# Performance work log

Hardware: AMD Instinct MI355X
Metric: run time of the kernel (lower is better)

Reference implementation:

```python
import jax, jax.numpy as jnp
import numpy as np

B = 32; N_NODES = 1000; WINDOW = 4; D = 128; N_PARTS = 10
T = 2; T_INT = 1; T_TEMP = 1
N_TOTAL = B * WINDOW * N_NODES
E_INT = 200000; E_TEMP = 96000


def setup_inputs() -> dict:
    key = jax.random.key(0)
    ks = jax.random.split(key, 24)
    inp = {}
    inp["node_inputs"] = jax.random.randint(ks[0], (B, N_NODES), 0, 10)
    inp["node_indices"] = jax.random.randint(ks[1], (E_INT,), 0, N_TOTAL)
    inp["neighbour_indices"] = jax.random.randint(ks[2], (E_INT,), 0, N_TOTAL)
    inp["temp_node_indices"] = jax.random.randint(ks[3], (E_TEMP,), 0, N_TOTAL)
    inp["temp_neighbour_indices"] = jax.random.randint(ks[4], (E_TEMP,), 0, N_TOTAL)

    def dense(k, din, dout):
        return jax.random.normal(k, (din, dout), jnp.float32) * np.float32(1.0 / np.sqrt(din))

    inp["embed_table"] = jax.random.normal(ks[5], (10, D), jnp.float32)
    # message MLP: 2*D -> 64 -> 64 -> 64 -> 64 -> D (4 gelu hidden, linear out)
    inp["msg_W_in"] = dense(ks[6], 2 * D, 64); inp["msg_b_in"] = jnp.zeros((64,), jnp.float32)
    inp["msg_W_hid"] = jax.random.normal(ks[7], (3, 64, 64), jnp.float32) * np.float32(1.0 / 8.0)
    inp["msg_b_hid"] = jnp.zeros((3, 64), jnp.float32)
    inp["msg_W_out"] = dense(ks[8], 64, D); inp["msg_b_out"] = jnp.zeros((D,), jnp.float32)
    # readout MLP: D -> 64 -> 64 -> 64 -> 64 -> n_parts
    inp["ro_W_in"] = dense(ks[9], D, 64); inp["ro_b_in"] = jnp.zeros((64,), jnp.float32)
    inp["ro_W_hid"] = jax.random.normal(ks[10], (3, 64, 64), jnp.float32) * np.float32(1.0 / 8.0)
    inp["ro_b_hid"] = jnp.zeros((3, 64), jnp.float32)
    inp["ro_W_out"] = dense(ks[11], 64, N_PARTS); inp["ro_b_out"] = jnp.zeros((N_PARTS,), jnp.float32)
    # GRU cells (tf.keras reset_after=True): kernel [D,3D], recurrent [D,3D], input+recurrent biases
    for nm, base in (("gi", 12), ("gt", 16)):
        inp[nm + "_Wx"] = dense(ks[base], D, 3 * D)
        inp[nm + "_Wh"] = dense(ks[base + 1], D, 3 * D)
        inp[nm + "_bi"] = jnp.zeros((3 * D,), jnp.float32)
        inp[nm + "_br"] = jnp.zeros((3 * D,), jnp.float32)
    return inp


def _mlp(x, W_in, b_in, W_hid, b_hid, W_out, b_out):
    h = jax.nn.gelu(x @ W_in + b_in, approximate=False)
    for i in range(W_hid.shape[0]):
        h = jax.nn.gelu(h @ W_hid[i] + b_hid[i], approximate=False)
    return h @ W_out + b_out


def _gru(h, x, Wx, Wh, bi, br):
    # tf.keras GRUCell, reset_after=True
    xz, xr, xh = jnp.split(x @ Wx + bi, 3, axis=1)
    hz, hr, hh = jnp.split(h @ Wh + br, 3, axis=1)
    z = jax.nn.sigmoid(xz + hz)
    r = jax.nn.sigmoid(xr + hr)
    cand = jnp.tanh(xh + r * hh)
    return z * h + (1.0 - z) * cand


def _message_mean(h, ni, bi, msg_p):
    g0 = h[ni]              # [E, D] node gather
    g1 = h[bi]              # [E, D] neighbour gather
    x = jnp.concatenate([jnp.concatenate([g0, g1], 1), jnp.concatenate([g1, g0], 1)], 0)  # [2E, 2D]
    msg = _mlp(x, *msg_p)   # [2E, D]
    seg = jnp.concatenate([bi, ni], 0)
    s = jax.ops.segment_sum(msg, seg, num_segments=h.shape[0])
    c = jax.ops.segment_sum(jnp.ones((seg.shape[0], 1), msg.dtype), seg, num_segments=h.shape[0])
    return s / jnp.maximum(c, 1.0)


def reference(node_inputs, node_indices, neighbour_indices, temp_node_indices, temp_neighbour_indices,
              embed_table, msg_W_in, msg_b_in, msg_W_hid, msg_b_hid, msg_W_out, msg_b_out,
              ro_W_in, ro_b_in, ro_W_hid, ro_b_hid, ro_W_out, ro_b_out,
              gi_Wx, gi_Wh, gi_bi, gi_br, gt_Wx, gt_Wh, gt_bi, gt_br):
    msg_p = (msg_W_in, msg_b_in, msg_W_hid, msg_b_hid, msg_W_out, msg_b_out)
    h = embed_table[node_inputs]                       # [B, N, D]
    h = jnp.repeat(h, WINDOW, axis=0).reshape(-1, D)   # [B*W*N, D]
    for _ in range(T):
        for _ in range(T_INT):
            m = _message_mean(h, node_indices, neighbour_indices, msg_p)
            h = _gru(h, m, gi_Wx, gi_Wh, gi_bi, gi_br)
        for _ in range(T_TEMP):
            m = _message_mean(h, temp_node_indices, temp_neighbour_indices, msg_p)
            h = _gru(h, m, gt_Wx, gt_Wh, gt_bi, gt_br)
    ridx = jnp.arange(N_NODES)[None, :] + jnp.arange(B)[:, None] * (WINDOW * N_NODES)
    return _mlp(h[ridx], ro_W_in, ro_b_in, ro_W_hid, ro_b_hid, ro_W_out, ro_b_out)  # [B, N, n_parts]
```

## Files before the change

kernel.cpp:

```cpp
#include <hip/hip_runtime.h>
#include <math.h>


#define DDIM 128
#define NTOT 128000
#define HBYTES 65536000ULL
#define EBLK 128

typedef unsigned short u16;
using f32x4 = __attribute__((ext_vector_type(4))) float;
using s16x8 = __attribute__((ext_vector_type(8))) short;

__device__ __forceinline__ float fast_rcp(float x) {
    return __builtin_amdgcn_rcpf(x);
}
__device__ __forceinline__ float gelu_fast(float x) {
    const float ax = fabsf(x) * 0.70710678118654752440f;
    const float t  = fast_rcp(1.0f + 0.3275911f * ax);
    const float poly = t * (0.254829592f + t * (-0.284496736f +
                       t * (1.421413741f + t * (-1.453152027f +
                       t * 1.061405429f))));
    const float e = __expf(-ax * ax);
    const float erfax = 1.0f - poly * e;
    const float erfv = copysignf(erfax, x);
    return 0.5f * x * (1.0f + erfv);
}
__device__ __forceinline__ float sigmoid_fast(float x) {
    return fast_rcp(1.0f + __expf(-x));
}
__device__ __forceinline__ float tanh_fast(float x) {
    const float e = __expf(2.0f * x);
    return 1.0f - 2.0f * fast_rcp(e + 1.0f);
}
__device__ __forceinline__ u16 f2bf(float x) {
    unsigned u = __float_as_uint(x);
    u += 0x7fffu + ((u >> 16) & 1u);
    return (u16)(u >> 16);
}
__device__ __forceinline__ float bf2f(u16 h) {
    return __uint_as_float(((unsigned)h) << 16);
}

__global__ __launch_bounds__(256) void embed_kernel(
    const int* __restrict__ inp, const float* __restrict__ table,
    float* __restrict__ h)
{
    int gid = blockIdx.x * 256 + threadIdx.x;
    if (gid >= NTOT * 32) return;
    int row = gid >> 5;
    int q   = gid & 31;
    int b   = row / 4000;
    int n   = (row % 4000) % 1000;
    int e   = inp[b * 1000 + n];
    ((float4*)h)[gid] = ((const float4*)table)[e * 32 + q];
}

__global__ __launch_bounds__(256) void hist_kernel(
    const int* __restrict__ ni, const int* __restrict__ bi, int E,
    int* __restrict__ deg)
{
    int g = blockIdx.x * 256 + threadIdx.x;
    if (g < E)          atomicAdd(&deg[bi[g]], 1);
    else if (g < 2 * E) atomicAdd(&deg[ni[g - E]], 1);
}

__global__ __launch_bounds__(256) void blockscan_kernel(
    const int* __restrict__ deg, int* __restrict__ offp, int* __restrict__ bsum)
{
    __shared__ int s[256];
    int tid = threadIdx.x;
    int i = blockIdx.x * 256 + tid;
    int v = deg[i];
    s[tid] = v;
    __syncthreads();
    for (int off = 1; off < 256; off <<= 1) {
        int t = (tid >= off) ? s[tid - off] : 0;
        __syncthreads();
        s[tid] += t;
        __syncthreads();
    }
    offp[i] = s[tid] - v;
    if (tid == 255) bsum[blockIdx.x] = s[255];
}

__global__ __launch_bounds__(512) void bscan_kernel(
    const int* __restrict__ bsum, int* __restrict__ bexc, int nb)
{
    __shared__ int s[512];
    int t = threadIdx.x;
    int v = (t < nb) ? bsum[t] : 0;
    s[t] = v;
    __syncthreads();
    for (int off = 1; off < 512; off <<= 1) {
        int u = (t >= off) ? s[t - off] : 0;
        __syncthreads();
        s[t] += u;
        __syncthreads();
    }
    if (t < nb) bexc[t] = s[t] - v;
}

__global__ __launch_bounds__(256) void fill_kernel(
    const int* __restrict__ ni, const int* __restrict__ bi, int E,
    const int* __restrict__ offp, const int* __restrict__ bexc,
    int* __restrict__ cursor, int* __restrict__ elist, int* __restrict__ slotseg)
{
    int g = blockIdx.x * 256 + threadIdx.x;
    if (g >= 2 * E) return;
    int seg = (g < E) ? bi[g] : ni[g - E];
    int pos = atomicAdd(&cursor[seg], 1);
    int slot = offp[seg] + bexc[seg >> 8] + pos;
    elist[slot] = g;
    slotseg[slot] = seg;
}

__global__ __launch_bounds__(256) void straddle_kernel(
    const int* __restrict__ slotseg, int nblocks32,
    int* __restrict__ list, int* __restrict__ count)
{
    int b = blockIdx.x * 256 + threadIdx.x + 1;
    if (b >= nblocks32) return;
    int s = slotseg[b * 32];
    if (s >= 0 && slotseg[b * 32 - 1] == s) {
        int pos = atomicAdd(count, 1);
        list[pos] = s;
    }
}

__global__ __launch_bounds__(64) void zero_rows_kernel(
    const int* __restrict__ list, const int* __restrict__ count,
    float* __restrict__ sbuf)
{
    int i = blockIdx.x;
    if (i >= *count) return;
    int seg = list[i];
    float4* row = (float4*)(sbuf + (size_t)seg * 64);
    if (threadIdx.x < 16) row[threadIdx.x] = make_float4(0.f, 0.f, 0.f, 0.f);
}


__global__ __launch_bounds__(256) void pack_gateBx_kernel(
    const float* __restrict__ Wout, const float* __restrict__ Wx,
    u16* __restrict__ BH, u16* __restrict__ BL)
{
    int idx = blockIdx.x * 256 + threadIdx.x;
    if (idx >= 24576) return;
    int j    = idx & 7;
    int lane = (idx >> 3) & 63;
    int tile = idx >> 9;
    int nt   = tile & 7;
    int g    = (tile >> 3) % 3;
    int kt   = tile / 24;
    int k   = kt * 32 + (lane >> 4) * 8 + j;
    int col = g * 128 + nt * 16 + (lane & 15);
    float acc = 0.0f;
    for (int t = 0; t < 128; ++t)
        acc = fmaf(Wout[k * 128 + t], Wx[t * 384 + col], acc);
    u16 hb = f2bf(acc);
    BH[idx] = hb;
    BL[idx] = f2bf(acc - bf2f(hb));
}

__global__ __launch_bounds__(256) void pack_gateBh_kernel(
    const float* __restrict__ Wh, u16* __restrict__ BH, u16* __restrict__ BL)
{
    int idx = blockIdx.x * 256 + threadIdx.x;
    if (idx >= 49152) return;
    int j    = idx & 7;
    int lane = (idx >> 3) & 63;
    int tile = idx >> 9;
    int nt   = tile & 7;
    int s    = (tile >> 3) % 3;
    int kt   = tile / 24;
    int k    = kt * 32 + (lane >> 4) * 8 + j;
    int col  = ((s == 2) ? 256 : s * 128) + nt * 16 + (lane & 15);
    float v = Wh[k * 384 + col];
    u16 hb = f2bf(v);
    BH[idx] = hb;
    BL[idx] = f2bf(v - bf2f(hb));
}

__global__ __launch_bounds__(256) void pack_gbias_kernel(
    const float* __restrict__ bout, const float* __restrict__ Wx,
    float* __restrict__ bc)
{
    int n = blockIdx.x * 256 + threadIdx.x;
    if (n >= 384) return;
    float acc = 0.0f;
    for (int t = 0; t < 128; ++t)
        acc = fmaf(bout[t], Wx[t * 384 + n], acc);
    bc[n] = acc;
}

__global__ __launch_bounds__(256) void pack_preB_kernel(
    const float* __restrict__ Win, u16* __restrict__ BH, u16* __restrict__ BL)
{
    int idx = blockIdx.x * 256 + threadIdx.x;
    if (idx >= 16384) return;
    int j    = idx & 7;
    int lane = (idx >> 3) & 63;
    int nt2  = (idx >> 9) & 7;
    int kt2  = idx >> 12;
    int k = kt2 * 32 + (lane >> 4) * 8 + j;
    int n = nt2 * 16 + (lane & 15);
    float v = (n < 64) ? Win[k * 64 + n] : Win[(128 + k) * 64 + (n - 64)];
    u16 hb = f2bf(v);
    BH[idx] = hb;
    BL[idx] = f2bf(v - bf2f(hb));
}

__global__ __launch_bounds__(256) void pack_hidB_kernel(
    const float* __restrict__ Whid, u16* __restrict__ BH, u16* __restrict__ BL)
{
    int idx = blockIdx.x * 256 + threadIdx.x;
    if (idx >= 12288) return;
    int j    = idx & 7;
    int lane = (idx >> 3) & 63;
    int nt   = (idx >> 9) & 3;
    int kt   = (idx >> 11) & 1;
    int L    = idx >> 12;
    int k = kt * 32 + (lane >> 4) * 8 + j;
    int n = nt * 16 + (lane & 15);
    float v = Whid[L * 4096 + k * 64 + n];
    u16 hb = f2bf(v);
    BH[idx] = hb;
    BL[idx] = f2bf(v - bf2f(hb));
}

__global__ __launch_bounds__(512, 2) void node_pre_mfma(
    const float* __restrict__ h,
    const u16* __restrict__ BpH, const u16* __restrict__ BpL,
    const float* __restrict__ binp, float* __restrict__ pout)
{
    __shared__ short sm[32768];
    const int tid  = threadIdx.x;
    const int lane = tid & 63;
    const int w    = tid >> 6;
    const int jg   = w & 1;
    const int mh   = w >> 1;
    const int nbase = blockIdx.x * 128;

    const int mS = tid >> 2, q = tid & 3;
    const int nodeS = nbase + mS;
    const int laneS = (mS & 15) + 16 * q;
    const int seg_m = mS >> 4;

    #pragma unroll
    for (int c = 0; c < 4; ++c) {
        const int kl = c * 32 + q * 8;
        const float* src = h + (size_t)nodeS * DDIM + kl;
        const float4 v0 = ((const float4*)src)[0];
        const float4 v1 = ((const float4*)src)[1];
        float xv[8] = { v0.x, v0.y, v0.z, v0.w, v1.x, v1.y, v1.z, v1.w };
        s16x8 hi8, lo8;
        #pragma unroll
        for (int i = 0; i < 8; ++i) {
            u16 hb = f2bf(xv[i]);
            hi8[i] = (short)hb;
            lo8[i] = (short)f2bf(xv[i] - bf2f(hb));
        }
        const int off = (c * 8 + seg_m) * 512 + laneS * 8;
        *(s16x8*)(sm + off)         = hi8;
        *(s16x8*)(sm + off + 16384) = lo8;
    }
    __syncthreads();

    f32x4 acc2[2][4];
    #pragma unroll
    for (int mf = 0; mf < 2; ++mf)
        #pragma unroll
        for (int t4 = 0; t4 < 4; ++t4)
            acc2[mf][t4] = (f32x4){0.f, 0.f, 0.f, 0.f};

    const s16x8* Ph8 = (const s16x8*)BpH;
    const s16x8* Pl8 = (const s16x8*)BpL;
    #pragma unroll
    for (int kt2 = 0; kt2 < 4; ++kt2) {
        const int a0off = (kt2 * 8 + 2 * mh) * 512 + lane * 8;
        const s16x8 aH0 = *(const s16x8*)(sm + a0off);
        const s16x8 aL0 = *(const s16x8*)(sm + 16384 + a0off);
        const s16x8 aH1 = *(const s16x8*)(sm + a0off + 512);
        const s16x8 aL1 = *(const s16x8*)(sm + 16384 + a0off + 512);
        #pragma unroll
        for (int t4 = 0; t4 < 4; ++t4) {
            const int idx = (kt2 * 8 + jg * 4 + t4) * 64 + lane;
            const s16x8 bH = Ph8[idx];
            const s16x8 bL = Pl8[idx];
            acc2[0][t4] = __builtin_amdgcn_mfma_f32_16x16x32_bf16(aH0, bH, acc2[0][t4], 0, 0, 0);
            acc2[0][t4] = __builtin_amdgcn_mfma_f32_16x16x32_bf16(aH0, bL, acc2[0][t4], 0, 0, 0);
            acc2[0][t4] = __builtin_amdgcn_mfma_f32_16x16x32_bf16(aL0, bH, acc2[0][t4], 0, 0, 0);
            acc2[1][t4] = __builtin_amdgcn_mfma_f32_16x16x32_bf16(aH1, bH, acc2[1][t4], 0, 0, 0);
            acc2[1][t4] = __builtin_amdgcn_mfma_f32_16x16x32_bf16(aH1, bL, acc2[1][t4], 0, 0, 0);
            acc2[1][t4] = __builtin_amdgcn_mfma_f32_16x16x32_bf16(aL1, bH, acc2[1][t4], 0, 0, 0);
        }
    }
    #pragma unroll
    for (int mf = 0; mf < 2; ++mf) {
        const int mtile = 2 * mh + mf;
        #pragma unroll
        for (int t4 = 0; t4 < 4; ++t4) {
            const int n = jg * 64 + t4 * 16 + (lane & 15);
            const float badd = (n < 64) ? binp[n] : 0.0f;
            #pragma unroll
            for (int r = 0; r < 4; ++r) {
                const int m = mtile * 16 + (lane >> 4) * 4 + r;
                pout[(size_t)(nbase + m) * DDIM + n] = acc2[mf][t4][r] + badd;
            }
        }
    }
}

__global__ __launch_bounds__(512) void edge_mlp_mfma(
    const int* __restrict__ ni, const int* __restrict__ bi, int E,
    const int* __restrict__ elist, const int* __restrict__ slotseg,
    const float* __restrict__ p,
    const u16* __restrict__ BhH, const u16* __restrict__ BhL,
    const float* __restrict__ bhid,
    float* __restrict__ sbuf)
{
    __shared__ short smA[17408];
    __shared__ int   segLDS[EBLK];
    __shared__ int   segedge[2];
    float* scat = (float*)smA;

    const int tid  = threadIdx.x;
    const int lane = tid & 63;
    const int w    = tid >> 6;
    const int s0   = blockIdx.x * EBLK;

    if (tid < 128) segLDS[tid] = slotseg[s0 + tid];
    if (tid == 0) segedge[0] = slotseg[s0 - 1];
    if (tid == 1) segedge[1] = slotseg[s0 + EBLK];

    {
        const int m  = (tid & 15) | (w << 4);
        const int gg = (tid >> 4) & 3;
        const int slot = s0 + m;
        const int g = elist[slot];
        int first, second;
        if (g < E) { first = ni[g];     second = bi[g];     }
        else       { first = bi[g - E]; second = ni[g - E]; }
        #pragma unroll
        for (int kt = 0; kt < 2; ++kt) {
            const int k0 = kt * 32 + gg * 8;
            const float4* pa = (const float4*)(p + (size_t)first  * DDIM + k0);
            const float4* pb = (const float4*)(p + (size_t)second * DDIM + 64 + k0);
            const float4 a0 = pa[0], a1 = pa[1], b0 = pb[0], b1 = pb[1];
            float x[8] = { a0.x + b0.x, a0.y + b0.y, a0.z + b0.z, a0.w + b0.w,
                           a1.x + b1.x, a1.y + b1.y, a1.z + b1.z, a1.w + b1.w };
            s16x8 hi8, lo8;
            #pragma unroll
            for (int j = 0; j < 8; ++j) {
                const float v = gelu_fast(x[j]);
                u16 hb = f2bf(v);
                hi8[j] = (short)hb;
                lo8[j] = (short)f2bf(v - bf2f(hb));
            }
            const int off = (kt * 8 + w) * 512 + lane * 8;
            *(s16x8*)(smA + off)        = hi8;
            *(s16x8*)(smA + 8192 + off) = lo8;
        }
    }

    const int mt = w;
    for (int L = 0; L < 2; ++L) {
        f32x4 acc[4];
        #pragma unroll
        for (int nt = 0; nt < 4; ++nt) {
            const float bv = bhid[L * 64 + nt * 16 + (lane & 15)];
            acc[nt] = (f32x4){bv, bv, bv, bv};
        }
        #pragma unroll
        for (int kt = 0; kt < 2; ++kt) {
            const s16x8 aH = *(const s16x8*)(smA + (kt * 8 + mt) * 512 + lane * 8);
            const s16x8 aL = *(const s16x8*)(smA + 8192 + (kt * 8 + mt) * 512 + lane * 8);
            #pragma unroll
            for (int nt = 0; nt < 4; ++nt) {
                const int bidx = (L * 8 + kt * 4 + nt) * 64 + lane;
                const s16x8 bH = ((const s16x8*)BhH)[bidx];
                const s16x8 bL = ((const s16x8*)BhL)[bidx];
                acc[nt] = __builtin_amdgcn_mfma_f32_16x16x32_bf16(aH, bH, acc[nt], 0, 0, 0);
                acc[nt] = __builtin_amdgcn_mfma_f32_16x16x32_bf16(aH, bL, acc[nt], 0, 0, 0);
                acc[nt] = __builtin_amdgcn_mfma_f32_16x16x32_bf16(aL, bH, acc[nt], 0, 0, 0);
            }
        }
        #pragma unroll
        for (int nt = 0; nt < 4; ++nt) {
            #pragma unroll
            for (int r = 0; r < 4; ++r) {
                const float v = gelu_fast(acc[nt][r]);
                const int ml  = (lane >> 4) * 4 + r;
                const int k   = nt * 16 + (lane & 15);
                const int kt2 = k >> 5, gg = (k >> 3) & 3, j = k & 7;
                const int off = (kt2 * 8 + mt) * 512 + (ml + 16 * gg) * 8 + j;
                u16 hb = f2bf(v);
                smA[off]        = (short)hb;
                smA[8192 + off] = (short)f2bf(v - bf2f(hb));
            }
        }
    }

    float gl[4][4];
    {
        f32x4 acc[4];
        #pragma unroll
        for (int nt = 0; nt < 4; ++nt) {
            const float bv = bhid[2 * 64 + nt * 16 + (lane & 15)];
            acc[nt] = (f32x4){bv, bv, bv, bv};
        }
        #pragma unroll
        for (int kt = 0; kt < 2; ++kt) {
            const s16x8 aH = *(const s16x8*)(smA + (kt * 8 + mt) * 512 + lane * 8);
            const s16x8 aL = *(const s16x8*)(smA + 8192 + (kt * 8 + mt) * 512 + lane * 8);
            #pragma unroll
            for (int nt = 0; nt < 4; ++nt) {
                const int bidx = (2 * 8 + kt * 4 + nt) * 64 + lane;
                const s16x8 bH = ((const s16x8*)BhH)[bidx];
                const s16x8 bL = ((const s16x8*)BhL)[bidx];
                acc[nt] = __builtin_amdgcn_mfma_f32_16x16x32_bf16(aH, bH, acc[nt], 0, 0, 0);
                acc[nt] = __builtin_amdgcn_mfma_f32_16x16x32_bf16(aH, bL, acc[nt], 0, 0, 0);
                acc[nt] = __builtin_amdgcn_mfma_f32_16x16x32_bf16(aL, bH, acc[nt], 0, 0, 0);
            }
        }
        #pragma unroll
        for (int nt = 0; nt < 4; ++nt)
            #pragma unroll
            for (int r = 0; r < 4; ++r)
                gl[nt][r] = gelu_fast(acc[nt][r]);
    }

    __syncthreads();
    #pragma unroll
    for (int nt = 0; nt < 4; ++nt)
        #pragma unroll
        for (int r = 0; r < 4; ++r)
            scat[(mt * 16 + (lane >> 4) * 4 + r) * 68 + nt * 16 + (lane & 15)]
                = gl[nt][r];
    __syncthreads();

    if (tid < 256) {
        const int col = tid & 63;
        const int r0  = (tid >> 6) * 32;
        const int r1  = r0 + 32;
        int   runSeg = -2;
        float runacc = 0.0f;
        bool  leftC  = true;
        for (int rowi = r0; rowi < r1; ++rowi) {
            const int sg = segLDS[rowi];
            const float v = scat[rowi * 68 + col];
            if (sg != runSeg) {
                if (runSeg >= 0) {
                    float* pp = sbuf + (size_t)runSeg * 64 + col;
                    if (leftC) *pp = runacc;
                    else       atomicAdd(pp, runacc);
                }
                runSeg = sg;
                runacc = v;
                if (rowi == r0) {
                    const int prev = (rowi == 0) ? segedge[0] : segLDS[rowi - 1];
                    leftC = (prev != sg);
                } else {
                    leftC = true;
                }
            } else {
                runacc += v;
            }
        }
        if (runSeg >= 0) {
            const int nxt = (r1 == 128) ? segedge[1] : segLDS[r1];
            const bool rightC = (nxt != runSeg);
            float* pp = sbuf + (size_t)runSeg * 64 + col;
            if (leftC && rightC) *pp = runacc;
            else                 atomicAdd(pp, runacc);
        }
    }
}

__global__ __launch_bounds__(256, 3) void gru_mfma_kernel(
    float* __restrict__ hio, const float* __restrict__ Ssum,
    const int* __restrict__ deg,
    const u16* __restrict__ BxH, const u16* __restrict__ BxL,
    const u16* __restrict__ BhH, const u16* __restrict__ BhL,
    const float* __restrict__ bc,
    const float* __restrict__ bi_, const float* __restrict__ br_,
    const u16* __restrict__ BpH, const u16* __restrict__ BpL,
    const float* __restrict__ binp,
    float* __restrict__ pout)
{
    __shared__ short sm[16384];
    const int tid  = threadIdx.x;
    const int lane = tid & 63;
    const int w    = tid >> 6;
    const int jg   = w & 1;
    const int mh   = w >> 1;
    const int nbase = blockIdx.x * 64;

    const int mS = tid >> 2, q = tid & 3;
    const int nodeS = nbase + mS;
    const int laneS = (mS & 15) + 16 * q;
    const int seg_m = mS >> 4;
    const int dg = deg[nodeS];
    const float ci = (dg > 0) ? fast_rcp((float)dg) : 0.0f;

    #pragma unroll
    for (int c = 0; c < 2; ++c) {
        const int kl = c * 32 + q * 8;
        const float* src = Ssum + (size_t)nodeS * 64 + kl;
        const float4 v0 = ((const float4*)src)[0];
        const float4 v1 = ((const float4*)src)[1];
        float xv[8] = { v0.x * ci, v0.y * ci, v0.z * ci, v0.w * ci,
                        v1.x * ci, v1.y * ci, v1.z * ci, v1.w * ci };
        s16x8 hi8, lo8;
        #pragma unroll
        for (int i = 0; i < 8; ++i) {
            u16 hb = f2bf(xv[i]);
            hi8[i] = (short)hb;
            lo8[i] = (short)f2bf(xv[i] - bf2f(hb));
        }
        const int off = (c * 4 + seg_m) * 512 + laneS * 8;
        *(s16x8*)(sm + off)        = hi8;
        *(s16x8*)(sm + off + 8192) = lo8;
    }
    __syncthreads();

    f32x4 acc[2][4][4];
    #pragma unroll
    for (int mf = 0; mf < 2; ++mf)
        #pragma unroll
        for (int g = 0; g < 4; ++g)
            #pragma unroll
            for (int t4 = 0; t4 < 4; ++t4)
                acc[mf][g][t4] = (f32x4){0.f, 0.f, 0.f, 0.f};

    {
        const s16x8* Bx8 = (const s16x8*)BxH;
        const s16x8* Bxl8 = (const s16x8*)BxL;
        #pragma unroll
        for (int kt = 0; kt < 2; ++kt) {
            const int a0off = (kt * 4 + 2 * mh) * 512 + lane * 8;
            const s16x8 aH0 = *(const s16x8*)(sm + a0off);
            const s16x8 aL0 = *(const s16x8*)(sm + 8192 + a0off);
            const s16x8 aH1 = *(const s16x8*)(sm + a0off + 512);
            const s16x8 aL1 = *(const s16x8*)(sm + 8192 + a0off + 512);
            #pragma unroll
            for (int g = 0; g < 3; ++g) {
                #pragma unroll
                for (int t4 = 0; t4 < 4; ++t4) {
                    const int idx = (kt * 24 + g * 8 + jg * 4 + t4) * 64 + lane;
                    const s16x8 bH = Bx8[idx];
                    const s16x8 bL = Bxl8[idx];
                    acc[0][g][t4] = __builtin_amdgcn_mfma_f32_16x16x32_bf16(aH0, bH, acc[0][g][t4], 0, 0, 0);
                    acc[0][g][t4] = __builtin_amdgcn_mfma_f32_16x16x32_bf16(aH0, bL, acc[0][g][t4], 0, 0, 0);
                    acc[0][g][t4] = __builtin_amdgcn_mfma_f32_16x16x32_bf16(aL0, bH, acc[0][g][t4], 0, 0, 0);
                    acc[1][g][t4] = __builtin_amdgcn_mfma_f32_16x16x32_bf16(aH1, bH, acc[1][g][t4], 0, 0, 0);
                    acc[1][g][t4] = __builtin_amdgcn_mfma_f32_16x16x32_bf16(aH1, bL, acc[1][g][t4], 0, 0, 0);
                    acc[1][g][t4] = __builtin_amdgcn_mfma_f32_16x16x32_bf16(aL1, bH, acc[1][g][t4], 0, 0, 0);
                }
            }
        }
    }
    __syncthreads();

    #pragma unroll
    for (int c = 0; c < 4; ++c) {
        const int kl = c * 32 + q * 8;
        const float* src = hio + (size_t)nodeS * DDIM + kl;
        const float4 v0 = ((const float4*)src)[0];
        const float4 v1 = ((const float4*)src)[1];
        float xv[8] = { v0.x, v0.y, v0.z, v0.w, v1.x, v1.y, v1.z, v1.w };
        s16x8 hi8, lo8;
        #pragma unroll
        for (int i = 0; i < 8; ++i) {
            u16 hb = f2bf(xv[i]);
            hi8[i] = (short)hb;
            lo8[i] = (short)f2bf(xv[i] - bf2f(hb));
        }
        const int off = (c * 4 + seg_m) * 512 + laneS * 8;
        *(s16x8*)(sm + off)        = hi8;
        *(s16x8*)(sm + off + 8192) = lo8;
    }
    __syncthreads();

    {
        const s16x8* Bh8 = (const s16x8*)BhH;
        const s16x8* Bhl8 = (const s16x8*)BhL;
        #pragma unroll
        for (int kt = 0; kt < 4; ++kt) {
            const int a0off = (kt * 4 + 2 * mh) * 512 + lane * 8;
            const s16x8 aH0 = *(const s16x8*)(sm + a0off);
            const s16x8 aL0 = *(const s16x8*)(sm + 8192 + a0off);
            const s16x8 aH1 = *(const s16x8*)(sm + a0off + 512);
            const s16x8 aL1 = *(const s16x8*)(sm + 8192 + a0off + 512);
            #pragma unroll
            for (int s = 0; s < 3; ++s) {
                const int g = (s == 2) ? 3 : s;
                #pragma unroll
                for (int t4 = 0; t4 < 4; ++t4) {
                    const int idx = (kt * 24 + s * 8 + jg * 4 + t4) * 64 + lane;
                    const s16x8 bH = Bh8[idx];
                    const s16x8 bL = Bhl8[idx];
                    acc[0][g][t4] = __builtin_amdgcn_mfma_f32_16x16x32_bf16(aH0, bH, acc[0][g][t4], 0, 0, 0);
                    acc[0][g][t4] = __builtin_amdgcn_mfma_f32_16x16x32_bf16(aH0, bL, acc[0][g][t4], 0, 0, 0);
                    acc[0][g][t4] = __builtin_amdgcn_mfma_f32_16x16x32_bf16(aL0, bH, acc[0][g][t4], 0, 0, 0);
                    acc[1][g][t4] = __builtin_amdgcn_mfma_f32_16x16x32_bf16(aH1, bH, acc[1][g][t4], 0, 0, 0);
                    acc[1][g][t4] = __builtin_amdgcn_mfma_f32_16x16x32_bf16(aH1, bL, acc[1][g][t4], 0, 0, 0);
                    acc[1][g][t4] = __builtin_amdgcn_mfma_f32_16x16x32_bf16(aL1, bH, acc[1][g][t4], 0, 0, 0);
                }
            }
        }
    }

    bool bon[2][4];
    #pragma unroll
    for (int mf = 0; mf < 2; ++mf)
        #pragma unroll
        for (int r = 0; r < 4; ++r)
            bon[mf][r] = deg[nbase + (2 * mh + mf) * 16 + (lane >> 4) * 4 + r] > 0;

    float hn[2][4][4];
    #pragma unroll
    for (int t4 = 0; t4 < 4; ++t4) {
        const int j = jg * 64 + t4 * 16 + (lane & 15);
        const float b_az = bi_[j]       + br_[j];
        const float b_ar = bi_[128 + j] + br_[128 + j];
        const float b_xh = bi_[256 + j];
        const float b_hh = br_[256 + j];
        const float bcz = bc[j];
        const float bcr = bc[128 + j];
        const float bcx = bc[256 + j];
        const int jbase = (j >> 5) * 2048 + ((j >> 3) & 3) * 128 + (j & 7);
        #pragma unroll
        for (int mf = 0; mf < 2; ++mf) {
            const int mtile = 2 * mh + mf;
            #pragma unroll
            for (int r = 0; r < 4; ++r) {
                const int m15 = (lane >> 4) * 4 + r;
                const int off = jbase + mtile * 512 + m15 * 8;
                const float hv = bf2f((u16)sm[off]) + bf2f((u16)sm[8192 + off]);
                const int m = mtile * 16 + m15;
                const float bsel = bon[mf][r] ? 1.0f : 0.0f;
                const float az = acc[mf][0][t4][r] + b_az + bsel * bcz;
                const float ar = acc[mf][1][t4][r] + b_ar + bsel * bcr;
                const float xh = acc[mf][2][t4][r] + b_xh + bsel * bcx;
                const float hh = acc[mf][3][t4][r] + b_hh;
                const float z    = sigmoid_fast(az);
                const float rr   = sigmoid_fast(ar);
                const float cand = tanh_fast(xh + rr * hh);
                const float v    = z * hv + (1.0f - z) * cand;
                hio[(size_t)(nbase + m) * DDIM + j] = v;
                hn[mf][t4][r] = v;
            }
        }
    }
    __syncthreads();

    #pragma unroll
    for (int mf = 0; mf < 2; ++mf) {
        const int mtile = 2 * mh + mf;
        #pragma unroll
        for (int t4 = 0; t4 < 4; ++t4) {
            #pragma unroll
            for (int r = 0; r < 4; ++r) {
                const int m15 = (lane >> 4) * 4 + r;
                const int j   = jg * 64 + t4 * 16 + (lane & 15);
                const int kt2 = j >> 5, gg = (j >> 3) & 3, jj = j & 7;
                const int off = (kt2 * 4 + mtile) * 512 + (m15 + 16 * gg) * 8 + jj;
                const float v = hn[mf][t4][r];
                u16 hb = f2bf(v);
                sm[off]        = (short)hb;
                sm[off + 8192] = (short)f2bf(v - bf2f(hb));
            }
        }
    }
    __syncthreads();

    f32x4 acc2[2][4];
    #pragma unroll
    for (int mf = 0; mf < 2; ++mf)
        #pragma unroll
        for (int t4 = 0; t4 < 4; ++t4)
            acc2[mf][t4] = (f32x4){0.f, 0.f, 0.f, 0.f};

    const s16x8* Ph8 = (const s16x8*)BpH;
    const s16x8* Pl8 = (const s16x8*)BpL;
    #pragma unroll
    for (int kt2 = 0; kt2 < 4; ++kt2) {
        const int a0off = (kt2 * 4 + 2 * mh) * 512 + lane * 8;
        const s16x8 aH0 = *(const s16x8*)(sm + a0off);
        const s16x8 aL0 = *(const s16x8*)(sm + 8192 + a0off);
        const s16x8 aH1 = *(const s16x8*)(sm + a0off + 512);
        const s16x8 aL1 = *(const s16x8*)(sm + 8192 + a0off + 512);
        #pragma unroll
        for (int t4 = 0; t4 < 4; ++t4) {
            const int idx = (kt2 * 8 + jg * 4 + t4) * 64 + lane;
            const s16x8 bH = Ph8[idx];
            const s16x8 bL = Pl8[idx];
            acc2[0][t4] = __builtin_amdgcn_mfma_f32_16x16x32_bf16(aH0, bH, acc2[0][t4], 0, 0, 0);
            acc2[0][t4] = __builtin_amdgcn_mfma_f32_16x16x32_bf16(aH0, bL, acc2[0][t4], 0, 0, 0);
            acc2[0][t4] = __builtin_amdgcn_mfma_f32_16x16x32_bf16(aL0, bH, acc2[0][t4], 0, 0, 0);
            acc2[1][t4] = __builtin_amdgcn_mfma_f32_16x16x32_bf16(aH1, bH, acc2[1][t4], 0, 0, 0);
            acc2[1][t4] = __builtin_amdgcn_mfma_f32_16x16x32_bf16(aH1, bL, acc2[1][t4], 0, 0, 0);
            acc2[1][t4] = __builtin_amdgcn_mfma_f32_16x16x32_bf16(aL1, bH, acc2[1][t4], 0, 0, 0);
        }
    }
    #pragma unroll
    for (int mf = 0; mf < 2; ++mf) {
        const int mtile = 2 * mh + mf;
        #pragma unroll
        for (int t4 = 0; t4 < 4; ++t4) {
            const int n = jg * 64 + t4 * 16 + (lane & 15);
            const float badd = (n < 64) ? binp[n] : 0.0f;
            #pragma unroll
            for (int r = 0; r < 4; ++r) {
                const int m = mtile * 16 + (lane >> 4) * 4 + r;
                pout[(size_t)(nbase + m) * DDIM + n] = acc2[mf][t4][r] + badd;
            }
        }
    }
}

__global__ __launch_bounds__(64) void readout_kernel(
    const float* __restrict__ h,
    const float* __restrict__ Win,  const float* __restrict__ bin,
    const float* __restrict__ Whid, const float* __restrict__ bhid,
    const float* __restrict__ Wout, const float* __restrict__ bout,
    float* __restrict__ out)
{
    __shared__ float xs[64 * 65];
    const int tid = threadIdx.x;
    const int row = blockIdx.x * 64 + tid;
    const int b = row / 1000, n = row % 1000;
    const float4* xrow = (const float4*)(h + ((size_t)b * 4000 + n) * DDIM);

    {
        float acc[64];
        #pragma unroll
        for (int j = 0; j < 64; ++j) acc[j] = bin[j];
        #pragma unroll 2
        for (int k4 = 0; k4 < 32; ++k4) {
            float4 xv = xrow[k4];
            #pragma unroll
            for (int kk = 0; kk < 4; ++kk) {
                const float xk = (&xv.x)[kk];
                const float* wr = Win + (size_t)(k4 * 4 + kk) * 64;
                #pragma unroll
                for (int j = 0; j < 64; ++j) acc[j] = fmaf(xk, wr[j], acc[j]);
            }
        }
        #pragma unroll
        for (int j = 0; j < 64; ++j) xs[tid * 65 + j] = gelu_fast(acc[j]);
    }

    for (int L = 0; L < 3; ++L) {
        float acc[64];
        #pragma unroll
        for (int j = 0; j < 64; ++j) acc[j] = bhid[L * 64 + j];
        #pragma unroll 4
        for (int k = 0; k < 64; ++k) {
            const float xk = xs[tid * 65 + k];
            const float* wr = Whid + (size_t)L * 4096 + (size_t)k * 64;
            #pragma unroll
            for (int j = 0; j < 64; ++j) acc[j] = fmaf(xk, wr[j], acc[j]);
        }
        #pragma unroll
        for (int j = 0; j < 64; ++j) xs[tid * 65 + j] = gelu_fast(acc[j]);
    }

    float acc[10];
    #pragma unroll
    for (int pj = 0; pj < 10; ++pj) acc[pj] = bout[pj];
    #pragma unroll 4
    for (int k = 0; k < 64; ++k) {
        const float xk = xs[tid * 65 + k];
        const float* wr = Wout + k * 10;
        #pragma unroll
        for (int pj = 0; pj < 10; ++pj) acc[pj] = fmaf(xk, wr[pj], acc[pj]);
    }
    #pragma unroll
    for (int pj = 0; pj < 10; ++pj) out[(size_t)row * 10 + pj] = acc[pj];
}

extern "C" void kernel_launch(void* const* d_in, const int* in_sizes, int n_in,
                              void* d_out, int out_size, void* d_ws, size_t ws_size,
                              hipStream_t stream) {
    const int*   node_inputs = (const int*)d_in[0];
    const int*   ni_int = (const int*)d_in[1];
    const int*   bi_int = (const int*)d_in[2];
    const int*   ni_tmp = (const int*)d_in[3];
    const int*   bi_tmp = (const int*)d_in[4];
    const float* embed  = (const float*)d_in[5];
    const float* mWin   = (const float*)d_in[6];
    const float* mbin   = (const float*)d_in[7];
    const float* mWhid  = (const float*)d_in[8];
    const float* mbhid  = (const float*)d_in[9];
    const float* mWout  = (const float*)d_in[10];
    const float* mbout  = (const float*)d_in[11];
    const float* roWin  = (const float*)d_in[12];
    const float* robin  = (const float*)d_in[13];
    const float* roWhid = (const float*)d_in[14];
    const float* robhid = (const float*)d_in[15];
    const float* roWout = (const float*)d_in[16];
    const float* robout = (const float*)d_in[17];
    const float* giWx = (const float*)d_in[18];
    const float* giWh = (const float*)d_in[19];
    const float* gibi = (const float*)d_in[20];
    const float* gibr = (const float*)d_in[21];
    const float* gtWx = (const float*)d_in[22];
    const float* gtWh = (const float*)d_in[23];
    const float* gtbi = (const float*)d_in[24];
    const float* gtbr = (const float*)d_in[25];
    float* out = (float*)d_out;

    const int E_INT = 200000, E_TMP = 96000;
    const int NSLOT_I = 400000;
    const int NSLOT_T = 192000;
    const int NBLK_I = NSLOT_I / EBLK;
    const int NBLK_T = NSLOT_T / EBLK;
    const int NS32_I = NSLOT_I / 32;
    const int NS32_T = NSLOT_T / 32;

    char* ws = (char*)d_ws;
    float* B0 = (float*)(ws);
    float* B1 = (float*)(ws + HBYTES);
    float* B2 = (float*)(ws + 2 * HBYTES);
    char*  ib = ws + 3 * HBYTES;

    int* deg_i   = (int*)(ib);
    int* deg_t   = (int*)(ib + 512000);
    int* offp_i  = (int*)(ib + 1024000);
    int* offp_t  = (int*)(ib + 1536000);
    int* bexc_i  = (int*)(ib + 2048000);
    int* bexc_t  = (int*)(ib + 2052096);
    int* bsum    = (int*)(ib + 2056192);
    int* cursor  = (int*)(ib + 2060288);
    int* el_i    = (int*)(ib + 2572288);
    int* el_t    = (int*)(ib + 4172288);
    int* ssi_raw = (int*)(ib + 4940288);
    int* sst_raw = (int*)(ib + 6540296);
    char* fb = ib + 8114176;
    u16* BxiH = (u16*)(fb);
    u16* BxiL = (u16*)(fb +  49152);
    u16* BhiH = (u16*)(fb +  98304);
    u16* BhiL = (u16*)(fb + 196608);
    u16* BxtH = (u16*)(fb + 294912);
    u16* BxtL = (u16*)(fb + 344064);
    u16* BhtH = (u16*)(fb + 393216);
    u16* BhtL = (u16*)(fb + 491520);
    float* bci = (float*)(fb + 589824);
    float* bct = (float*)(fb + 591360);
    u16* BpH  = (u16*)(fb + 592896);
    u16* BpL  = (u16*)(fb + 625664);
    u16* EhH  = (u16*)(fb + 658432);
    u16* EhL  = (u16*)(fb + 683008);
    int* str_i  = (int*)(fb + 707584);
    int* str_t  = (int*)(fb + 757584);
    int* strc_i = (int*)(fb + 781584);
    int* strc_t = (int*)(fb + 781588);
    int* ssi = ssi_raw + 1;
    int* sst = sst_raw + 1;

    embed_kernel<<<16000, 256, 0, stream>>>(node_inputs, embed, B0);

    hipMemsetAsync(deg_i, 0, NTOT * sizeof(int), stream);
    hipMemsetAsync(deg_t, 0, NTOT * sizeof(int), stream);
    hist_kernel<<<(2 * E_INT + 255) / 256, 256, 0, stream>>>(ni_int, bi_int, E_INT, deg_i);
    hist_kernel<<<(2 * E_TMP + 255) / 256, 256, 0, stream>>>(ni_tmp, bi_tmp, E_TMP, deg_t);

    hipMemsetAsync(ssi_raw, 0xFF, (size_t)(NSLOT_I + 2) * sizeof(int), stream);
    hipMemsetAsync(sst_raw, 0xFF, (size_t)(NSLOT_T + 2) * sizeof(int), stream);

    blockscan_kernel<<<500, 256, 0, stream>>>(deg_i, offp_i, bsum);
    bscan_kernel<<<1, 512, 0, stream>>>(bsum, bexc_i, 500);
    hipMemsetAsync(cursor, 0, NTOT * sizeof(int), stream);
    fill_kernel<<<(2 * E_INT + 255) / 256, 256, 0, stream>>>(
        ni_int, bi_int, E_INT, offp_i, bexc_i, cursor, el_i, ssi);

    blockscan_kernel<<<500, 256, 0, stream>>>(deg_t, offp_t, bsum);
    bscan_kernel<<<1, 512, 0, stream>>>(bsum, bexc_t, 500);
    hipMemsetAsync(cursor, 0, NTOT * sizeof(int), stream);
    fill_kernel<<<(2 * E_TMP + 255) / 256, 256, 0, stream>>>(
        ni_tmp, bi_tmp, E_TMP, offp_t, bexc_t, cursor, el_t, sst);

    hipMemsetAsync(strc_i, 0, sizeof(int), stream);
    hipMemsetAsync(strc_t, 0, sizeof(int), stream);
    straddle_kernel<<<(NS32_I + 255) / 256, 256, 0, stream>>>(ssi, NS32_I, str_i, strc_i);
    straddle_kernel<<<(NS32_T + 255) / 256, 256, 0, stream>>>(sst, NS32_T, str_t, strc_t);

    pack_gateBx_kernel<<<96, 256, 0, stream>>>(mWout, giWx, BxiH, BxiL);
    pack_gateBx_kernel<<<96, 256, 0, stream>>>(mWout, gtWx, BxtH, BxtL);
    pack_gateBh_kernel<<<192, 256, 0, stream>>>(giWh, BhiH, BhiL);
    pack_gateBh_kernel<<<192, 256, 0, stream>>>(gtWh, BhtH, BhtL);
    pack_gbias_kernel<<<2, 256, 0, stream>>>(mbout, giWx, bci);
    pack_gbias_kernel<<<2, 256, 0, stream>>>(mbout, gtWx, bct);
    pack_preB_kernel<<<64, 256, 0, stream>>>(mWin, BpH, BpL);
    pack_hidB_kernel<<<48, 256, 0, stream>>>(mWhid, EhH, EhL);

    node_pre_mfma<<<NTOT / 128, 512, 0, stream>>>(B0, BpH, BpL, mbin, B1);

    for (int ph = 0; ph < 4; ++ph) {
        const bool isInt = (ph % 2 == 0);
        if (isInt) {
            zero_rows_kernel<<<NS32_I, 64, 0, stream>>>(str_i, strc_i, B2);
            edge_mlp_mfma<<<NBLK_I, 512, 0, stream>>>(
                ni_int, bi_int, E_INT, el_i, ssi, B1,
                EhH, EhL, mbhid, B2);
            gru_mfma_kernel<<<NTOT / 64, 256, 0, stream>>>(
                B0, B2, deg_i, BxiH, BxiL, BhiH, BhiL, bci,
                gibi, gibr, BpH, BpL, mbin, B1);
        } else {
            zero_rows_kernel<<<NS32_T, 64, 0, stream>>>(str_t, strc_t, B2);
            edge_mlp_mfma<<<NBLK_T, 512, 0, stream>>>(
                ni_tmp, bi_tmp, E_TMP, el_t, sst, B1,
                EhH, EhL, mbhid, B2);
            gru_mfma_kernel<<<NTOT / 64, 256, 0, stream>>>(
                B0, B2, deg_t, BxtH, BxtL, BhtH, BhtL, bct,
                gtbi, gtbr, BpH, BpL, mbin, B1);
        }
    }

    readout_kernel<<<500, 64, 0, stream>>>(
        B0, roWin, robin, roWhid, robhid, roWout, robout, out);
}
```

Before: 1.253 ms.

## Merge first half of recurrent GEMM into input phase and stage output through LDS

The GRU kernel now loads the first half of the hidden state together with the message sums, so the first MFMA phase also runs the first two K-tiles of the recurrent GEMM. The second phase handles only the remaining two K-tiles, and the gate epilogue picks the LDS region by column group. This overlaps more global loads with compute and shortens the serialized second load-and-sync phase. The projection output is also written to a padded LDS tile and stored as row-contiguous float4s rather than scattered scalar stores, at the cost of an extra barrier and slightly more shared memory.

Measured after the change: 1.314 ms. +4.9%, slower.

```diff
diff --git a/kernel.cpp b/kernel.cpp
--- a/kernel.cpp
+++ b/kernel.cpp
@@ -487,7 +487,7 @@
     const float* __restrict__ binp,
     float* __restrict__ pout)
 {
-    __shared__ short sm[16384];
+    __shared__ short sm[16768];
     const int tid  = threadIdx.x;
     const int lane = tid & 63;
     const int w    = tid >> 6;
@@ -502,24 +502,46 @@
     const int dg = deg[nodeS];
     const float ci = (dg > 0) ? fast_rcp((float)dg) : 0.0f;
 
-    #pragma unroll
-    for (int c = 0; c < 2; ++c) {
-        const int kl = c * 32 + q * 8;
-        const float* src = Ssum + (size_t)nodeS * 64 + kl;
-        const float4 v0 = ((const float4*)src)[0];
-        const float4 v1 = ((const float4*)src)[1];
-        float xv[8] = { v0.x * ci, v0.y * ci, v0.z * ci, v0.w * ci,
-                        v1.x * ci, v1.y * ci, v1.z * ci, v1.w * ci };
-        s16x8 hi8, lo8;
-        #pragma unroll
-        for (int i = 0; i < 8; ++i) {
-            u16 hb = f2bf(xv[i]);
-            hi8[i] = (short)hb;
-            lo8[i] = (short)f2bf(xv[i] - bf2f(hb));
-        }
-        const int off = (c * 4 + seg_m) * 512 + laneS * 8;
-        *(s16x8*)(sm + off)        = hi8;
-        *(s16x8*)(sm + off + 8192) = lo8;
+    {
+        float4 sv[4], hv0[4];
+        #pragma unroll
+        for (int c = 0; c < 2; ++c) {
+            const int kl = c * 32 + q * 8;
+            sv[c * 2]     = ((const float4*)(Ssum + (size_t)nodeS * 64 + kl))[0];
+            sv[c * 2 + 1] = ((const float4*)(Ssum + (size_t)nodeS * 64 + kl))[1];
+            hv0[c * 2]     = ((const float4*)(hio + (size_t)nodeS * DDIM + kl))[0];
+            hv0[c * 2 + 1] = ((const float4*)(hio + (size_t)nodeS * DDIM + kl))[1];
+        }
+        #pragma unroll
+        for (int c = 0; c < 2; ++c) {
+            float xv[8] = { sv[c*2].x * ci, sv[c*2].y * ci, sv[c*2].z * ci, sv[c*2].w * ci,
+                            sv[c*2+1].x * ci, sv[c*2+1].y * ci, sv[c*2+1].z * ci, sv[c*2+1].w * ci };
+            s16x8 hi8, lo8;
+            #pragma unroll
+            for (int i = 0; i < 8; ++i) {
+                u16 hb = f2bf(xv[i]);
+                hi8[i] = (short)hb;
+                lo8[i] = (short)f2bf(xv[i] - bf2f(hb));
+            }
+            const int off = (c * 4 + seg_m) * 512 + laneS * 8;
+            *(s16x8*)(sm + off)        = hi8;
+            *(s16x8*)(sm + off + 8192) = lo8;
+        }
+        #pragma unroll
+        for (int c = 0; c < 2; ++c) {
+            float xv[8] = { hv0[c*2].x, hv0[c*2].y, hv0[c*2].z, hv0[c*2].w,
+                            hv0[c*2+1].x, hv0[c*2+1].y, hv0[c*2+1].z, hv0[c*2+1].w };
+            s16x8 hi8, lo8;
+            #pragma unroll
+            for (int i = 0; i < 8; ++i) {
+                u16 hb = f2bf(xv[i]);
+                hi8[i] = (short)hb;
+                lo8[i] = (short)f2bf(xv[i] - bf2f(hb));
+            }
+            const int off = 4096 + (c * 4 + seg_m) * 512 + laneS * 8;
+            *(s16x8*)(sm + off)        = hi8;
+            *(s16x8*)(sm + off + 8192) = lo8;
+        }
     }
     __syncthreads();
 
@@ -535,34 +557,61 @@
     {
         const s16x8* Bx8 = (const s16x8*)BxH;
         const s16x8* Bxl8 = (const s16x8*)BxL;
+        const s16x8* Bh8 = (const s16x8*)BhH;
+        const s16x8* Bhl8 = (const s16x8*)BhL;
         #pragma unroll
         for (int kt = 0; kt < 2; ++kt) {
-            const int a0off = (kt * 4 + 2 * mh) * 512 + lane * 8;
-            const s16x8 aH0 = *(const s16x8*)(sm + a0off);
-            const s16x8 aL0 = *(const s16x8*)(sm + 8192 + a0off);
-            const s16x8 aH1 = *(const s16x8*)(sm + a0off + 512);
-            const s16x8 aL1 = *(const s16x8*)(sm + 8192 + a0off + 512);
-            #pragma unroll
-            for (int g = 0; g < 3; ++g) {
+            {
+                const int a0off = (kt * 4 + 2 * mh) * 512 + lane * 8;
+                const s16x8 aH0 = *(const s16x8*)(sm + a0off);
+                const s16x8 aL0 = *(const s16x8*)(sm + 8192 + a0off);
+                const s16x8 aH1 = *(const s16x8*)(sm + a0off + 512);
+                const s16x8 aL1 = *(const s16x8*)(sm + 8192 + a0off + 512);
                 #pragma unroll
-                for (int t4 = 0; t4 < 4; ++t4) {
-                    const int idx = (kt * 24 + g * 8 + jg * 4 + t4) * 64 + lane;
-                    const s16x8 bH = Bx8[idx];
-                    const s16x8 bL = Bxl8[idx];
-                    acc[0][g][t4] = __builtin_amdgcn_mfma_f32_16x16x32_bf16(aH0, bH, acc[0][g][t4], 0, 0, 0);
-                    acc[0][g][t4] = __builtin_amdgcn_mfma_f32_16x16x32_bf16(aH0, bL, acc[0][g][t4], 0, 0, 0);
-                    acc[0][g][t4] = __builtin_amdgcn_mfma_f32_16x16x32_bf16(aL0, bH, acc[0][g][t4], 0, 0, 0);
-                    acc[1][g][t4] = __builtin_amdgcn_mfma_f32_16x16x32_bf16(aH1, bH, acc[1][g][t4], 0, 0, 0);
-                    acc[1][g][t4] = __builtin_amdgcn_mfma_f32_16x16x32_bf16(aH1, bL, acc[1][g][t4], 0, 0, 0);
-                    acc[1][g][t4] = __builtin_amdgcn_mfma_f32_16x16x32_bf16(aL1, bH, acc[1][g][t4], 0, 0, 0);
+                for (int g = 0; g < 3; ++g) {
+                    #pragma unroll
+                    for (int t4 = 0; t4 < 4; ++t4) {
+                        const int idx = (kt * 24 + g * 8 + jg * 4 + t4) * 64 + lane;
+                        const s16x8 bH = Bx8[idx];
+                        const s16x8 bL = Bxl8[idx];
+                        acc[0][g][t4] = __builtin_amdgcn_mfma_f32_16x16x32_bf16(aH0, bH, acc[0][g][t4], 0, 0, 0);
+                        acc[0][g][t4] = __builtin_amdgcn_mfma_f32_16x16x32_bf16(aH0, bL, acc[0][g][t4], 0, 0, 0);
+                        acc[0][g][t4] = __builtin_amdgcn_mfma_f32_16x16x32_bf16(aL0, bH, acc[0][g][t4], 0, 0, 0);
+                        acc[1][g][t4] = __builtin_amdgcn_mfma_f32_16x16x32_bf16(aH1, bH, acc[1][g][t4], 0, 0, 0);
+                        acc[1][g][t4] = __builtin_amdgcn_mfma_f32_16x16x32_bf16(aH1, bL, acc[1][g][t4], 0, 0, 0);
+                        acc[1][g][t4] = __builtin_amdgcn_mfma_f32_16x16x32_bf16(aL1, bH, acc[1][g][t4], 0, 0, 0);
+                    }
                 }
             }
-        }
-    }
-    __syncthreads();
-
-    #pragma unroll
-    for (int c = 0; c < 4; ++c) {
+            {
+                const int a0off = 4096 + (kt * 4 + 2 * mh) * 512 + lane * 8;
+                const s16x8 aH0 = *(const s16x8*)(sm + a0off);
+                const s16x8 aL0 = *(const s16x8*)(sm + 8192 + a0off);
+                const s16x8 aH1 = *(const s16x8*)(sm + a0off + 512);
+                const s16x8 aL1 = *(const s16x8*)(sm + 8192 + a0off + 512);
+                #pragma unroll
+                for (int s = 0; s < 3; ++s) {
+                    const int g = (s == 2) ? 3 : s;
+                    #pragma unroll
+                    for (int t4 = 0; t4 < 4; ++t4) {
+                        const int idx = (kt * 24 + s * 8 + jg * 4 + t4) * 64 + lane;
+                        const s16x8 bH = Bh8[idx];
+                        const s16x8 bL = Bhl8[idx];
+                        acc[0][g][t4] = __builtin_amdgcn_mfma_f32_16x16x32_bf16(aH0, bH, acc[0][g][t4], 0, 0, 0);
+                        acc[0][g][t4] = __builtin_amdgcn_mfma_f32_16x16x32_bf16(aH0, bL, acc[0][g][t4], 0, 0, 0);
+                        acc[0][g][t4] = __builtin_amdgcn_mfma_f32_16x16x32_bf16(aL0, bH, acc[0][g][t4], 0, 0, 0);
+                        acc[1][g][t4] = __builtin_amdgcn_mfma_f32_16x16x32_bf16(aH1, bH, acc[1][g][t4], 0, 0, 0);
+                        acc[1][g][t4] = __builtin_amdgcn_mfma_f32_16x16x32_bf16(aH1, bL, acc[1][g][t4], 0, 0, 0);
+                        acc[1][g][t4] = __builtin_amdgcn_mfma_f32_16x16x32_bf16(aL1, bH, acc[1][g][t4], 0, 0, 0);
+                    }
+                }
+            }
+        }
+    }
+    __syncthreads();
+
+    #pragma unroll
+    for (int c = 2; c < 4; ++c) {
         const int kl = c * 32 + q * 8;
         const float* src = hio + (size_t)nodeS * DDIM + kl;
         const float4 v0 = ((const float4*)src)[0];
@@ -575,7 +624,7 @@
             hi8[i] = (short)hb;
             lo8[i] = (short)f2bf(xv[i] - bf2f(hb));
         }
-        const int off = (c * 4 + seg_m) * 512 + laneS * 8;
+        const int off = ((c - 2) * 4 + seg_m) * 512 + laneS * 8;
         *(s16x8*)(sm + off)        = hi8;
         *(s16x8*)(sm + off + 8192) = lo8;
     }
@@ -585,8 +634,8 @@
         const s16x8* Bh8 = (const s16x8*)BhH;
         const s16x8* Bhl8 = (const s16x8*)BhL;
         #pragma unroll
-        for (int kt = 0; kt < 4; ++kt) {
-            const int a0off = (kt * 4 + 2 * mh) * 512 + lane * 8;
+        for (int kt = 2; kt < 4; ++kt) {
+            const int a0off = ((kt - 2) * 4 + 2 * mh) * 512 + lane * 8;
             const s16x8 aH0 = *(const s16x8*)(sm + a0off);
             const s16x8 aL0 = *(const s16x8*)(sm + 8192 + a0off);
             const s16x8 aH1 = *(const s16x8*)(sm + a0off + 512);
@@ -617,10 +666,12 @@
         for (int r = 0; r < 4; ++r)
             bon[mf][r] = deg[nbase + (2 * mh + mf) * 16 + (lane >> 4) * 4 + r] > 0;
 
+    const int regbase = jg ? 0 : 4096;
     float hn[2][4][4];
     #pragma unroll
     for (int t4 = 0; t4 < 4; ++t4) {
         const int j = jg * 64 + t4 * 16 + (lane & 15);
+        const int jj = j & 63;
         const float b_az = bi_[j]       + br_[j];
         const float b_ar = bi_[128 + j] + br_[128 + j];
         const float b_xh = bi_[256 + j];
@@ -628,7 +679,7 @@
         const float bcz = bc[j];
         const float bcr = bc[128 + j];
         const float bcx = bc[256 + j];
-        const int jbase = (j >> 5) * 2048 + ((j >> 3) & 3) * 128 + (j & 7);
+        const int jbase = regbase + (jj >> 5) * 2048 + ((jj >> 3) & 3) * 128 + (jj & 7);
         #pragma unroll
         for (int mf = 0; mf < 2; ++mf) {
             const int mtile = 2 * mh + mf;
@@ -703,19 +754,31 @@
             acc2[1][t4] = __builtin_amdgcn_mfma_f32_16x16x32_bf16(aL1, bH, acc2[1][t4], 0, 0, 0);
         }
     }
-    #pragma unroll
-    for (int mf = 0; mf < 2; ++mf) {
-        const int mtile = 2 * mh + mf;
-        #pragma unroll
-        for (int t4 = 0; t4 < 4; ++t4) {
-            const int n = jg * 64 + t4 * 16 + (lane & 15);
-            const float badd = (n < 64) ? binp[n] : 0.0f;
-            #pragma unroll
-            for (int r = 0; r < 4; ++r) {
-                const int m = mtile * 16 + (lane >> 4) * 4 + r;
-                pout[(size_t)(nbase + m) * DDIM + n] = acc2[mf][t4][r] + badd;
-            }
-        }
+    __syncthreads();
+
+    {
+        float* pf = (float*)sm;
+        #pragma unroll
+        for (int mf = 0; mf < 2; ++mf) {
+            const int mtile = 2 * mh + mf;
+            #pragma unroll
+            for (int t4 = 0; t4 < 4; ++t4) {
+                const int n = jg * 64 + t4 * 16 + (lane & 15);
+                const float badd = (n < 64) ? binp[n] : 0.0f;
+                #pragma unroll
+                for (int r = 0; r < 4; ++r) {
+                    const int m = mtile * 16 + (lane >> 4) * 4 + r;
+                    pf[m * 130 + n] = acc2[mf][t4][r] + badd;
+                }
+            }
+        }
+        __syncthreads();
+        const int prow = tid >> 2, pcol = (tid & 3) * 32;
+        float4* dst = (float4*)(pout + (size_t)(nbase + prow) * DDIM + pcol);
+        const float* srcr = pf + prow * 130 + pcol;
+        #pragma unroll
+        for (int qq = 0; qq < 8; ++qq)
+            dst[qq] = make_float4(srcr[qq*4], srcr[qq*4+1], srcr[qq*4+2], srcr[qq*4+3]);
     }
 }
 
```
